# Kernel optimization log

Hardware: AMD Instinct MI355X
Metric: run time of the kernel (lower is better)

Reference implementation:

```python
import jax, jax.numpy as jnp
import numpy as np

SUP_NUM = 2048
EPS_NORM = 1e-12
EPS_BN = 1e-5


def l2norm(v, axis):
    n = jnp.sqrt(jnp.sum(v * v, axis=axis, keepdims=True))
    return v / jnp.maximum(n, EPS_NORM)


def segment_mean(vals, ids, num_segments):
    # vals: [N, C], ids: [N] int -> [num_segments, C]
    s = jax.ops.segment_sum(vals, ids, num_segments=num_segments)
    cnt = jax.ops.segment_sum(jnp.ones((vals.shape[0],), vals.dtype), ids, num_segments=num_segments)
    return s / jnp.maximum(cnt, 1.0)[:, None]


def setup_inputs() -> dict:
    key = jax.random.key(0)
    ks = jax.random.split(key, 6)
    B, Cin, H, W = 1, 3, 1024, 1024
    Cf = 32
    x = jax.random.normal(ks[0], (B, Cin, H, W), dtype=jnp.float32)
    conv_feat = jax.random.normal(ks[1], (B, Cf, H, W), dtype=jnp.float32)
    vit_feature = jax.random.normal(ks[2], (B, SUP_NUM, Cf), dtype=jnp.float32)
    seg_ids = jax.random.randint(ks[3], (B * H * W,), 0, SUP_NUM, dtype=jnp.int32)
    w_soft = jax.random.normal(ks[4], (1, 2 * Cf, 3), dtype=jnp.float32) * 0.1
    b_soft = jnp.zeros((1,), jnp.float32)
    bn_gamma = jnp.ones((1,), jnp.float32)
    bn_beta = jnp.zeros((1,), jnp.float32)
    return {"x": x, "conv_feat": conv_feat, "vit_feature": vit_feature, "seg_ids": seg_ids,
            "w_soft": w_soft, "b_soft": b_soft, "bn_gamma": bn_gamma, "bn_beta": bn_beta}


def reference(x, conv_feat, vit_feature, seg_ids, w_soft, b_soft, bn_gamma, bn_beta):
    B, Cf, H, W = conv_feat.shape
    Cin = x.shape[1]
    # F.normalize(conv, p=2, dim=1)
    conv_1 = l2norm(conv_feat, axis=1)
    # [B,C,H,W] -> [B*H*W, C]
    F1 = conv_1.transpose(0, 2, 3, 1).reshape(-1, Cf)
    X = jax.lax.stop_gradient(x).transpose(0, 2, 3, 1).reshape(-1, Cin)
    # superpixel scatter-mean (replaces the per-segment Python loop)
    M_F = segment_mean(F1, seg_ids, SUP_NUM)                  # [Sup, Cf]
    X_F = segment_mean(X, seg_ids, SUP_NUM)                   # [Sup, Cin]
    M_F = M_F.reshape(B, SUP_NUM, Cf)
    X_F = X_F.reshape(B, SUP_NUM, Cin).transpose(0, 2, 1)     # [B, Cin, Sup]
    vit_n = l2norm(vit_feature, axis=-1)
    all_F = jnp.concatenate([M_F, vit_n], axis=-1).transpose(0, 2, 1)  # [B, 2Cf, Sup]
    all_F = l2norm(all_F, axis=1)
    # Conv1d(2Cf -> 1, k=3, pad=1)
    z = jax.lax.conv_general_dilated(all_F, w_soft, window_strides=(1,), padding=((1, 1),),
                                     dimension_numbers=("NCH", "OIH", "NCH")) + b_soft[None, :, None]
    # BatchNorm1d (training-mode batch stats over (B, L))
    mu = jnp.mean(z, axis=(0, 2), keepdims=True)
    var = jnp.mean((z - mu) ** 2, axis=(0, 2), keepdims=True)
    z = bn_gamma[None, :, None] * (z - mu) / jnp.sqrt(var + EPS_BN) + bn_beta[None, :, None]
    result = jax.nn.sigmoid(z)                                # [B, 1, Sup]
    gap = jnp.mean(result, axis=-1, keepdims=True)            # AdaptiveAvgPool1d(1)
    return (result, gap, all_F, X_F)
```

## Files before the change

### kernel.cpp

```cpp
#include <hip/hip_runtime.h>
#include <hip/hip_bf16.h>
#include <hip/hip_fp16.h>

#define SUP 2048
#define NB  256

#define SC_CONV 1024.0f
#define SC_X0   512.0f
#define SC_XLO  256.0f
#define ISC_CONV (1.0f/1024.0f)
#define ISC_X0   (1.0f/512.0f)
#define ISC_XLO  (1.0f/256.0f)

__device__ __forceinline__ int enc2i(int qa, int qb) {
    return ((qa - (qb < 0 ? 1 : 0)) << 16) + (qb & 0xFFFF);
}
__device__ __forceinline__ int enc2f(float a, float b) {
    return enc2i(__float2int_rn(a), __float2int_rn(b));
}

__global__ __launch_bounds__(512) void k_segfused(const float* __restrict__ conv,
                                                  const float* __restrict__ x,
                                                  const int* __restrict__ ids,
                                                  float* __restrict__ accum,
                                                  __half* __restrict__ pbuf,
                                                  int npix) {
    __shared__ int sacc[18 * SUP];
    for (int i = threadIdx.x; i < 18 * SUP; i += blockDim.x) sacc[i] = 0;
    __syncthreads();

    int per = (npix + (int)gridDim.x - 1) / (int)gridDim.x;
    int start = blockIdx.x * per;
    int end = min(start + per, npix);

    for (int p = start + (int)threadIdx.x; p < end; p += (int)blockDim.x) {
        int s = ids[p];
        float cv[32];
        float ss = 0.f;
#pragma unroll
        for (int c = 0; c < 32; ++c) {
            cv[c] = conv[(size_t)c * npix + p];
        }
        float x0 = x[p];
        float x1 = x[(size_t)npix + p];
        float x2 = x[(size_t)2 * npix + p];
#pragma unroll
        for (int c = 0; c < 32; ++c) ss += cv[c] * cv[c];
        float iv = 1.0f / fmaxf(sqrtf(ss), 1e-12f);
        float sc = iv * SC_CONV;
#pragma unroll
        for (int r = 0; r < 16; ++r) {
            atomicAdd(&sacc[r * SUP + s],
                      enc2f(cv[2 * r] * sc, cv[2 * r + 1] * sc));
        }
        atomicAdd(&sacc[16 * SUP + s], enc2f(x0 * SC_X0, x1 * SC_XLO));
        atomicAdd(&sacc[17 * SUP + s], enc2i(1, __float2int_rn(x2 * SC_XLO)));
    }
    __syncthreads();

    for (int i = threadIdx.x; i < 18 * SUP; i += blockDim.x) {
        int S = sacc[i];
        int qb = (int)(short)(S & 0xFFFF);
        int qa = (S - qb) >> 16;
        int row = i >> 11;
        int s = i & (SUP - 1);
        int hi_row, lo_row;
        float fhi, flo;
        if (row < 16) {
            hi_row = 2 * row; lo_row = 2 * row + 1;
            fhi = (float)qa * ISC_CONV;
            flo = (float)qb * ISC_CONV;
        } else if (row == 16) {
            hi_row = 32; lo_row = 33;
            fhi = (float)qa * ISC_X0;
            flo = (float)qb * ISC_XLO;
        } else {
            hi_row = 35; lo_row = 34;
            fhi = (float)qa;
            flo = (float)qb * ISC_XLO;
        }
        if (pbuf) {
            __half* dst = pbuf + (size_t)blockIdx.x * 36 * SUP;
            dst[hi_row * SUP + s] = __float2half(fhi);
            dst[lo_row * SUP + s] = __float2half(flo);
        } else {
            unsafeAtomicAdd(&accum[hi_row * SUP + s], fhi);
            unsafeAtomicAdd(&accum[lo_row * SUP + s], flo);
        }
    }
}

__global__ __launch_bounds__(256) void k_reduce(const __half* __restrict__ pbuf,
                                                float* __restrict__ accum) {
    int j8 = (blockIdx.x * blockDim.x + threadIdx.x) * 8;
    if (j8 >= 36 * SUP) return;
    float s[8];
#pragma unroll
    for (int k = 0; k < 8; ++k) s[k] = 0.f;
    for (int b = 0; b < NB; ++b) {
        uint4 u = *(const uint4*)(pbuf + (size_t)b * 36 * SUP + j8);
        __half2 h0 = *reinterpret_cast<__half2*>(&u.x);
        __half2 h1 = *reinterpret_cast<__half2*>(&u.y);
        __half2 h2 = *reinterpret_cast<__half2*>(&u.z);
        __half2 h3 = *reinterpret_cast<__half2*>(&u.w);
        float2 f0 = __half22float2(h0), f1 = __half22float2(h1);
        float2 f2 = __half22float2(h2), f3 = __half22float2(h3);
        s[0] += f0.x; s[1] += f0.y; s[2] += f1.x; s[3] += f1.y;
        s[4] += f2.x; s[5] += f2.y; s[6] += f3.x; s[7] += f3.y;
    }
    float4 o0 = {s[0], s[1], s[2], s[3]};
    float4 o1 = {s[4], s[5], s[6], s[7]};
    *(float4*)(accum + j8) = o0;
    *(float4*)(accum + j8 + 4) = o1;
}

__device__ __forceinline__ void compute_col(const float* __restrict__ accum,
                                            const float* __restrict__ vit,
                                            int g, float* __restrict__ col) {
    if (g < 0 || g >= SUP) {
#pragma unroll
        for (int c = 0; c < 64; ++c) col[c] = 0.f;
        return;
    }
    float cnt = fmaxf(accum[35 * SUP + g], 1.0f);
    float rc = 1.0f / cnt;
#pragma unroll
    for (int c = 0; c < 32; ++c) col[c] = accum[c * SUP + g] * rc;
    float vs = 0.f;
#pragma unroll
    for (int c = 0; c < 32; ++c) {
        float v = vit[g * 32 + c];
        col[32 + c] = v;
        vs += v * v;
    }
    float vinv = 1.0f / fmaxf(sqrtf(vs), 1e-12f);
#pragma unroll
    for (int c = 0; c < 32; ++c) col[32 + c] *= vinv;
    float ssq = 0.f;
#pragma unroll
    for (int c = 0; c < 64; ++c) ssq += col[c] * col[c];
    float ainv = 1.0f / fmaxf(sqrtf(ssq), 1e-12f);
#pragma unroll
    for (int c = 0; c < 64; ++c) col[c] *= ainv;
}

__global__ __launch_bounds__(256) void k_finalconv(const float* __restrict__ accum,
                                                   const float* __restrict__ vit,
                                                   const float* __restrict__ w,
                                                   const float* __restrict__ bias,
                                                   float* __restrict__ allF_out,
                                                   float* __restrict__ xf_out,
                                                   float* __restrict__ z_out) {
    __shared__ float L[258][65];
    __shared__ float sw[192];
    int t = threadIdx.x;
    int b0 = blockIdx.x * 256;
    if (t < 192) sw[t] = w[t];

    float col[64];
    int g = b0 + t;
    compute_col(accum, vit, g, col);
#pragma unroll
    for (int c = 0; c < 64; ++c) L[t + 1][c] = col[c];
#pragma unroll
    for (int c = 0; c < 64; ++c) allF_out[c * SUP + g] = col[c];
    {
        float cnt = fmaxf(accum[35 * SUP + g], 1.0f);
        float rc = 1.0f / cnt;
#pragma unroll
        for (int c = 0; c < 3; ++c)
            xf_out[c * SUP + g] = accum[(32 + c) * SUP + g] * rc;
    }
    if (t == 0) {
        compute_col(accum, vit, b0 - 1, col);
#pragma unroll
        for (int c = 0; c < 64; ++c) L[0][c] = col[c];
    }
    if (t == 255) {
        compute_col(accum, vit, b0 + 256, col);
#pragma unroll
        for (int c = 0; c < 64; ++c) L[257][c] = col[c];
    }
    __syncthreads();

    float acc = bias[0];
#pragma unroll
    for (int c = 0; c < 64; ++c) {
        acc += sw[c * 3] * L[t][c] + sw[c * 3 + 1] * L[t + 1][c]
             + sw[c * 3 + 2] * L[t + 2][c];
    }
    z_out[b0 + t] = acc;
}

__global__ __launch_bounds__(512) void k_head2(const float* __restrict__ z,
                                               const float* __restrict__ gamma,
                                               const float* __restrict__ beta,
                                               float* __restrict__ out) {
    __shared__ float red[8];
    __shared__ float bc[2];
    int tid = threadIdx.x;
    int lane = tid & 63, wid = tid >> 6;

    float zs[4];
#pragma unroll
    for (int j = 0; j < 4; ++j) zs[j] = z[j * 512 + tid];

    float s1 = zs[0] + zs[1] + zs[2] + zs[3];
#pragma unroll
    for (int o = 32; o > 0; o >>= 1) s1 += __shfl_down(s1, o);
    if (lane == 0) red[wid] = s1;
    __syncthreads();
    if (tid == 0) {
        float t = 0.f;
        for (int i = 0; i < 8; ++i) t += red[i];
        bc[0] = t / (float)SUP;
    }
    __syncthreads();
    float mu = bc[0];

    float s2 = 0.f;
#pragma unroll
    for (int j = 0; j < 4; ++j) { float d = zs[j] - mu; s2 += d * d; }
#pragma unroll
    for (int o = 32; o > 0; o >>= 1) s2 += __shfl_down(s2, o);
    __syncthreads();
    if (lane == 0) red[wid] = s2;
    __syncthreads();
    if (tid == 0) {
        float t = 0.f;
        for (int i = 0; i < 8; ++i) t += red[i];
        bc[1] = t / (float)SUP;
    }
    __syncthreads();
    float var = bc[1];

    float invstd = rsqrtf(var + 1e-5f);
    float gm = gamma[0], bt = beta[0];
    float gsum = 0.f;
#pragma unroll
    for (int j = 0; j < 4; ++j) {
        int p = j * 512 + tid;
        float zn = gm * (zs[j] - mu) * invstd + bt;
        float r = 1.0f / (1.0f + expf(-zn));
        out[p] = r;
        gsum += r;
    }
#pragma unroll
    for (int o = 32; o > 0; o >>= 1) gsum += __shfl_down(gsum, o);
    __syncthreads();
    if (lane == 0) red[wid] = gsum;
    __syncthreads();
    if (tid == 0) {
        float t = 0.f;
        for (int i = 0; i < 8; ++i) t += red[i];
        out[SUP] = t / (float)SUP;
    }
}

extern "C" void kernel_launch(void* const* d_in, const int* in_sizes, int n_in,
                              void* d_out, int out_size, void* d_ws, size_t ws_size,
                              hipStream_t stream) {
    const float* x     = (const float*)d_in[0];
    const float* conv  = (const float*)d_in[1];
    const float* vit   = (const float*)d_in[2];
    const int*   ids   = (const int*)d_in[3];
    const float* w     = (const float*)d_in[4];
    const float* b     = (const float*)d_in[5];
    const float* gamma = (const float*)d_in[6];
    const float* beta  = (const float*)d_in[7];
    float* out = (float*)d_out;

    int npix = in_sizes[3];

    float* accum = (float*)d_ws;
    float* zbuf = accum + 36 * SUP;
    __half* pbuf = (__half*)(zbuf + SUP);

    size_t need = (36 * SUP + SUP) * sizeof(float)
                + (size_t)NB * 36 * SUP * sizeof(__half);
    bool useP = ws_size >= need;

    if (!useP) hipMemsetAsync(accum, 0, 36 * SUP * sizeof(float), stream);

    k_segfused<<<NB, 512, 0, stream>>>(conv, x, ids, accum,
                                       useP ? pbuf : (__half*)nullptr, npix);
    if (useP) {
        k_reduce<<<(36 * SUP / 8 + 255) / 256, 256, 0, stream>>>(pbuf, accum);
    }

    float* allF = out + SUP + 1;
    float* xf = allF + 64 * SUP;
    k_finalconv<<<SUP / 256, 256, 0, stream>>>(accum, vit, w, b, allF, xf, zbuf);

    k_head2<<<1, 512, 0, stream>>>(zbuf, gamma, beta, out);
}
```

Measured before the change: 79.99 us.

## Pack four fixed-point channels per 64-bit LDS atomic and vectorize pixel loads

Replaces the packing of two 16-bit fixed-point channels per 32-bit LDS atomic with four 16-bit lanes per 64-bit atomic. This halves the atomic count per pixel from 18 to 9. Each thread now handles four consecutive pixels with float4/int4 loads and a scalar tail loop, which cuts global load instructions. The cost is less headroom per 16-bit lane, since x is now scaled by 128 instead of 512/256, which risks overflow or precision loss when many pixels fall in one segment within a block. The shared buffer stays the same size (9 x 2048 x 8 bytes).

Result: no change. 79.08 us (-1.1%).

```diff
diff --git a/kernel.cpp b/kernel.cpp
--- a/kernel.cpp
+++ b/kernel.cpp
@@ -6,18 +6,15 @@
 #define NB  256
 
 #define SC_CONV 1024.0f
-#define SC_X0   512.0f
-#define SC_XLO  256.0f
+#define SC_X    128.0f
 #define ISC_CONV (1.0f/1024.0f)
-#define ISC_X0   (1.0f/512.0f)
-#define ISC_XLO  (1.0f/256.0f)
-
-__device__ __forceinline__ int enc2i(int qa, int qb) {
-    return ((qa - (qb < 0 ? 1 : 0)) << 16) + (qb & 0xFFFF);
-}
-__device__ __forceinline__ int enc2f(float a, float b) {
-    return enc2i(__float2int_rn(a), __float2int_rn(b));
-}
+#define ISC_X    (1.0f/128.0f)
+
+__device__ __forceinline__ long long enc4(int qa, int qb, int qc, int qd) {
+    return ((long long)qa << 48) + ((long long)qb << 32)
+         + ((long long)qc << 16) + (long long)qd;
+}
+__device__ __forceinline__ int q(float v) { return __float2int_rn(v); }
 
 __global__ __launch_bounds__(512) void k_segfused(const float* __restrict__ conv,
                                                   const float* __restrict__ x,
@@ -25,67 +22,116 @@
                                                   float* __restrict__ accum,
                                                   __half* __restrict__ pbuf,
                                                   int npix) {
-    __shared__ int sacc[18 * SUP];
-    for (int i = threadIdx.x; i < 18 * SUP; i += blockDim.x) sacc[i] = 0;
-    __syncthreads();
-
-    int per = (npix + (int)gridDim.x - 1) / (int)gridDim.x;
+    __shared__ unsigned long long sacc[9 * SUP];
+    for (int i = threadIdx.x; i < 9 * SUP; i += blockDim.x) sacc[i] = 0ULL;
+    __syncthreads();
+
+    int per = ((npix + (int)gridDim.x - 1) / (int)gridDim.x + 3) & ~3;
     int start = blockIdx.x * per;
     int end = min(start + per, npix);
-
-    for (int p = start + (int)threadIdx.x; p < end; p += (int)blockDim.x) {
+    int nvec = (end > start) ? ((end - start) & ~3) : 0;
+    int vend = start + nvec;
+
+    for (int p = start + (int)threadIdx.x * 4; p < vend; p += (int)blockDim.x * 4) {
+        int4 id4 = *(const int4*)(ids + p);
+        float4 cv[32];
+#pragma unroll
+        for (int c = 0; c < 32; ++c)
+            cv[c] = *(const float4*)(conv + (size_t)c * npix + p);
+        float4 xa = *(const float4*)(x + p);
+        float4 xb = *(const float4*)(x + (size_t)npix + p);
+        float4 xc = *(const float4*)(x + (size_t)2 * npix + p);
+
+        float4 ss = {0.f, 0.f, 0.f, 0.f};
+#pragma unroll
+        for (int c = 0; c < 32; ++c) {
+            ss.x += cv[c].x * cv[c].x;
+            ss.y += cv[c].y * cv[c].y;
+            ss.z += cv[c].z * cv[c].z;
+            ss.w += cv[c].w * cv[c].w;
+        }
+        float s0 = SC_CONV / fmaxf(sqrtf(ss.x), 1e-12f);
+        float s1 = SC_CONV / fmaxf(sqrtf(ss.y), 1e-12f);
+        float s2 = SC_CONV / fmaxf(sqrtf(ss.z), 1e-12f);
+        float s3 = SC_CONV / fmaxf(sqrtf(ss.w), 1e-12f);
+
+#pragma unroll
+        for (int r = 0; r < 8; ++r) {
+            const float4 c0 = cv[4 * r], c1 = cv[4 * r + 1];
+            const float4 c2 = cv[4 * r + 2], c3 = cv[4 * r + 3];
+            atomicAdd(&sacc[r * SUP + id4.x],
+                (unsigned long long)enc4(q(c0.x * s0), q(c1.x * s0), q(c2.x * s0), q(c3.x * s0)));
+            atomicAdd(&sacc[r * SUP + id4.y],
+                (unsigned long long)enc4(q(c0.y * s1), q(c1.y * s1), q(c2.y * s1), q(c3.y * s1)));
+            atomicAdd(&sacc[r * SUP + id4.z],
+                (unsigned long long)enc4(q(c0.z * s2), q(c1.z * s2), q(c2.z * s2), q(c3.z * s2)));
+            atomicAdd(&sacc[r * SUP + id4.w],
+                (unsigned long long)enc4(q(c0.w * s3), q(c1.w * s3), q(c2.w * s3), q(c3.w * s3)));
+        }
+        atomicAdd(&sacc[8 * SUP + id4.x],
+            (unsigned long long)enc4(1, q(xa.x * SC_X), q(xb.x * SC_X), q(xc.x * SC_X)));
+        atomicAdd(&sacc[8 * SUP + id4.y],
+            (unsigned long long)enc4(1, q(xa.y * SC_X), q(xb.y * SC_X), q(xc.y * SC_X)));
+        atomicAdd(&sacc[8 * SUP + id4.z],
+            (unsigned long long)enc4(1, q(xa.z * SC_X), q(xb.z * SC_X), q(xc.z * SC_X)));
+        atomicAdd(&sacc[8 * SUP + id4.w],
+            (unsigned long long)enc4(1, q(xa.w * SC_X), q(xb.w * SC_X), q(xc.w * SC_X)));
+    }
+    for (int p = vend + (int)threadIdx.x; p < end; p += (int)blockDim.x) {
         int s = ids[p];
-        float cv[32];
+        float cvv[32];
         float ss = 0.f;
 #pragma unroll
         for (int c = 0; c < 32; ++c) {
-            cv[c] = conv[(size_t)c * npix + p];
+            cvv[c] = conv[(size_t)c * npix + p];
+            ss += cvv[c] * cvv[c];
         }
-        float x0 = x[p];
-        float x1 = x[(size_t)npix + p];
-        float x2 = x[(size_t)2 * npix + p];
-#pragma unroll
-        for (int c = 0; c < 32; ++c) ss += cv[c] * cv[c];
-        float iv = 1.0f / fmaxf(sqrtf(ss), 1e-12f);
-        float sc = iv * SC_CONV;
-#pragma unroll
-        for (int r = 0; r < 16; ++r) {
+        float sc = SC_CONV / fmaxf(sqrtf(ss), 1e-12f);
+#pragma unroll
+        for (int r = 0; r < 8; ++r)
             atomicAdd(&sacc[r * SUP + s],
-                      enc2f(cv[2 * r] * sc, cv[2 * r + 1] * sc));
-        }
-        atomicAdd(&sacc[16 * SUP + s], enc2f(x0 * SC_X0, x1 * SC_XLO));
-        atomicAdd(&sacc[17 * SUP + s], enc2i(1, __float2int_rn(x2 * SC_XLO)));
-    }
-    __syncthreads();
-
-    for (int i = threadIdx.x; i < 18 * SUP; i += blockDim.x) {
-        int S = sacc[i];
+                (unsigned long long)enc4(q(cvv[4 * r] * sc), q(cvv[4 * r + 1] * sc),
+                                         q(cvv[4 * r + 2] * sc), q(cvv[4 * r + 3] * sc)));
+        atomicAdd(&sacc[8 * SUP + s],
+            (unsigned long long)enc4(1, q(x[p] * SC_X),
+                                     q(x[(size_t)npix + p] * SC_X),
+                                     q(x[(size_t)2 * npix + p] * SC_X)));
+    }
+    __syncthreads();
+
+    for (int i = threadIdx.x; i < 9 * SUP; i += blockDim.x) {
+        long long S = (long long)sacc[i];
+        int qd = (int)(short)(S & 0xFFFF); S = (S - qd) >> 16;
+        int qc = (int)(short)(S & 0xFFFF); S = (S - qc) >> 16;
         int qb = (int)(short)(S & 0xFFFF);
-        int qa = (S - qb) >> 16;
+        int qa = (int)((S - qb) >> 16);
         int row = i >> 11;
         int s = i & (SUP - 1);
-        int hi_row, lo_row;
-        float fhi, flo;
-        if (row < 16) {
-            hi_row = 2 * row; lo_row = 2 * row + 1;
-            fhi = (float)qa * ISC_CONV;
-            flo = (float)qb * ISC_CONV;
-        } else if (row == 16) {
-            hi_row = 32; lo_row = 33;
-            fhi = (float)qa * ISC_X0;
-            flo = (float)qb * ISC_XLO;
-        } else {
-            hi_row = 35; lo_row = 34;
-            fhi = (float)qa;
-            flo = (float)qb * ISC_XLO;
-        }
         if (pbuf) {
             __half* dst = pbuf + (size_t)blockIdx.x * 36 * SUP;
-            dst[hi_row * SUP + s] = __float2half(fhi);
-            dst[lo_row * SUP + s] = __float2half(flo);
+            if (row < 8) {
+                dst[(4 * row + 0) * SUP + s] = __float2half((float)qa * ISC_CONV);
+                dst[(4 * row + 1) * SUP + s] = __float2half((float)qb * ISC_CONV);
+                dst[(4 * row + 2) * SUP + s] = __float2half((float)qc * ISC_CONV);
+                dst[(4 * row + 3) * SUP + s] = __float2half((float)qd * ISC_CONV);
+            } else {
+                dst[35 * SUP + s] = __float2half((float)qa);
+                dst[32 * SUP + s] = __float2half((float)qb * ISC_X);
+                dst[33 * SUP + s] = __float2half((float)qc * ISC_X);
+                dst[34 * SUP + s] = __float2half((float)qd * ISC_X);
+            }
         } else {
-            unsafeAtomicAdd(&accum[hi_row * SUP + s], fhi);
-            unsafeAtomicAdd(&accum[lo_row * SUP + s], flo);
+            if (row < 8) {
+                unsafeAtomicAdd(&accum[(4 * row + 0) * SUP + s], (float)qa * ISC_CONV);
+                unsafeAtomicAdd(&accum[(4 * row + 1) * SUP + s], (float)qb * ISC_CONV);
+                unsafeAtomicAdd(&accum[(4 * row + 2) * SUP + s], (float)qc * ISC_CONV);
+                unsafeAtomicAdd(&accum[(4 * row + 3) * SUP + s], (float)qd * ISC_CONV);
+            } else {
+                unsafeAtomicAdd(&accum[35 * SUP + s], (float)qa);
+                unsafeAtomicAdd(&accum[32 * SUP + s], (float)qb * ISC_X);
+                unsafeAtomicAdd(&accum[33 * SUP + s], (float)qc * ISC_X);
+                unsafeAtomicAdd(&accum[34 * SUP + s], (float)qd * ISC_X);
+            }
         }
     }
 }
```
